# Optimization experiments

Hardware: AMD Instinct MI355X
Metric: run time of the kernel (lower is better)

The kernel has to match this reference:

```python
import jax, jax.numpy as jnp
import numpy as np

CUTOFF = 8.0
N_NODES = 100000
N_EDGES = 3200000
HIDDEN = 256
VOCAB = 178


def _swish(x):
    return x * jax.nn.sigmoid(x)


def _safe_norm(v):
    # L2 norm over last axis with torch-style zero subgradient at 0
    ss = jnp.sum(v * v, axis=-1)
    return jnp.where(ss == 0, 0.0, jnp.sqrt(jnp.where(ss == 0, 1.0, ss)))


def _safe_atan2(b, a):
    # atan2 with finite grad at (0,0); forward value identical (atan2(0,0)=0)
    deg = (a == 0) & (b == 0)
    return jnp.arctan2(b, jnp.where(deg, 1.0, a))


def _scatter_argmin(d, idx, num_seg):
    # replicates torch_scatter.scatter_min argmin output (empty segments -> 0)
    E = d.shape[0]
    mn = jax.ops.segment_min(d, idx, num_segments=num_seg)
    cand = jnp.where(d == mn[idx], jnp.arange(E), E)
    am = jax.ops.segment_min(cand, idx, num_segments=num_seg)
    return jnp.where(am >= E, 0, am)


def _dist_calc(cutoff, vecs, dist, i, j, num_nodes):
    argmin0 = _scatter_argmin(dist, i, num_nodes)
    n0 = j[argmin0]
    dist1 = dist + jnp.zeros_like(dist).at[argmin0].set(cutoff)
    argmin1 = _scatter_argmin(dist1, i, num_nodes)
    n1 = j[argmin1]
    argmin0_j = _scatter_argmin(dist, j, num_nodes)
    n0_j = i[argmin0_j]
    dist1_j = dist + jnp.zeros_like(dist).at[argmin0_j].set(cutoff)
    argmin1_j = _scatter_argmin(dist1_j, j, num_nodes)
    n1_j = i[argmin1_j]

    n0 = n0[i]
    n1 = n1[i]
    n0_j = n0_j[j]
    n1_j = n1_j[j]

    idx_iref = jnp.where(n0 == j, argmin1[i], argmin0[i])
    idx_jref = jnp.where(n0_j == i, argmin1_j[j], argmin0_j[j])

    pos_ji = vecs                      # [E,3]
    pos_in0 = vecs[argmin0[i]]         # vecs[argmin0][i]
    pos_in1 = vecs[argmin1[i]]
    pos_iref = vecs[idx_iref]
    pos_jref_j = vecs[idx_jref]

    a = jnp.sum(-pos_ji * pos_in0, axis=-1)
    b = _safe_norm(jnp.cross(-pos_ji, pos_in0))
    theta = _safe_atan2(b, a)
    theta = jnp.where(theta < 0, theta + jnp.pi, theta)

    dist_ji = _safe_norm(pos_ji)

    plane1 = jnp.cross(-pos_ji, pos_in0)
    plane2 = jnp.cross(-pos_ji, pos_in1)
    a = jnp.sum(plane1 * plane2, axis=-1)
    b = jnp.sum(jnp.cross(plane1, plane2) * pos_ji, axis=-1) / dist_ji
    phi = _safe_atan2(b, a)
    phi = jnp.where(phi < 0, phi + jnp.pi, phi)

    plane1 = jnp.cross(pos_ji, pos_jref_j)
    plane2 = jnp.cross(pos_ji, pos_iref)
    a = jnp.sum(plane1 * plane2, axis=-1)
    b = jnp.sum(jnp.cross(plane1, plane2) * pos_ji, axis=-1) / dist_ji
    tau = _safe_atan2(b, a)
    tau = jnp.where(tau < 0, tau + jnp.pi, tau)

    return dist, theta, phi, tau


def setup_inputs() -> dict:
    key = jax.random.key(0)
    k1, k2, k3, k4, k5 = jax.random.split(key, 5)
    x = jax.random.randint(k1, (N_NODES,), 0, VOCAB)
    pos = jax.random.normal(k2, (N_NODES, 3), jnp.float32) * 3.0
    i = jax.random.randint(k3, (N_EDGES,), 0, N_NODES)
    off = jax.random.randint(k4, (N_EDGES,), 1, N_NODES)
    j = (i + off) % N_NODES  # no self-edges -> dist > 0
    edge_index = jnp.stack([i, j])
    emb_weight = jax.random.normal(k5, (VOCAB, HIDDEN), jnp.float32)
    return {"x": x, "pos": pos, "edge_index": edge_index, "emb_weight": emb_weight}


def reference(x, pos, edge_index, emb_weight):
    i, j = edge_index[0], edge_index[1]
    vecs = pos[j] - pos[i]          # [E,3]
    dist = _safe_norm(vecs)         # [E]
    h = _swish(emb_weight[x])       # [N,H]
    dist, theta, phi, tau = _dist_calc(CUTOFF, vecs, dist, i, j, pos.shape[0])
    return h, dist, theta, phi, tau
```

## Files before the change

### kernel.cpp

```cpp
#include <hip/hip_runtime.h>
#include <math.h>

#define HID 256
#define PI_F 3.14159265358979323846f
typedef unsigned long long ull;

struct F3 { float x, y, z; };

__device__ __forceinline__ F3 crossc(F3 a, F3 b) {
    F3 r;
    float t1 = a.z * b.y;
    r.x = __builtin_fmaf(a.y, b.z, -t1);
    float t2 = a.x * b.z;
    r.y = __builtin_fmaf(a.z, b.x, -t2);
    float t3 = a.y * b.x;
    r.z = __builtin_fmaf(a.x, b.y, -t3);
    return r;
}
__device__ __forceinline__ float dotf(F3 a, F3 b) {
#pragma clang fp contract(off)
    float px = a.x * b.x;
    float py = a.y * b.y;
    float pz = a.z * b.z;
    return (px + py) + pz;
}
__device__ __forceinline__ float sqrt_cr(float ss) {
    return (float)sqrt((double)ss);
}
__device__ __forceinline__ float safe_atan2(float b, float a) {
    float aa = (a == 0.f && b == 0.f) ? 1.f : a;
    return atan2f(b, aa);
}
__device__ __forceinline__ F3 loadp(const float* __restrict__ pos, int n) {
    F3 r;
    r.x = pos[3 * n + 0];
    r.y = pos[3 * n + 1];
    r.z = pos[3 * n + 2];
    return r;
}
__device__ __forceinline__ F3 subv(F3 a, F3 b) {
#pragma clang fp contract(off)
    F3 r;
    r.x = a.x - b.x;
    r.y = a.y - b.y;
    r.z = a.z - b.z;
    return r;
}
__device__ __forceinline__ ull umin64(ull a, ull b) { return a < b ? a : b; }
__device__ __forceinline__ ull umax64(ull a, ull b) { return a > b ? a : b; }

__device__ __forceinline__ void insert2(ull* __restrict__ s, unsigned db, ull key) {
    unsigned hi2 = ((const unsigned*)s)[3];
    if (db > hi2) return;
    unsigned hi1 = ((const unsigned*)s)[1];
    if (db <= hi1) {
        ull ret = atomicMin(&s[0], key);
        ull loser = umax64(ret, key);
        if (loser != ~0ull) atomicMin(&s[1], loser);
    } else {
        atomicMin(&s[1], key);
    }
}

__global__ void k_pass1(const int* __restrict__ ei, const int* __restrict__ ej,
                        const float* __restrict__ pos, float* __restrict__ dist,
                        ull* __restrict__ slotsA, ull* __restrict__ slotsB,
                        const unsigned* __restrict__ thrA, const unsigned* __restrict__ thrB,
                        int e0, int e1) {
#pragma clang fp contract(off)
    int e = e0 + blockIdx.x * blockDim.x + threadIdx.x;
    if (e >= e1) return;
    int ii = ei[e], jj = ej[e];
    F3 v = subv(loadp(pos, jj), loadp(pos, ii));
    float sx = v.x * v.x;
    float sy = v.y * v.y;
    float sz = v.z * v.z;
    float ss = (sx + sy) + sz;
    float d = (ss == 0.f) ? 0.f : sqrt_cr(ss);
    dist[e] = d;
    unsigned db = __float_as_uint(d);
    ull key = ((ull)db << 32) | (unsigned)e;
    if (db <= thrA[ii]) insert2(&slotsA[2 * (size_t)ii], db, key);
    if (db <= thrB[jj]) insert2(&slotsB[2 * (size_t)jj], db, key);
}

__global__ void k_snapshot(const ull* __restrict__ slotsA, const ull* __restrict__ slotsB,
                           unsigned* __restrict__ thrA, unsigned* __restrict__ thrB, int N) {
    int n = blockIdx.x * blockDim.x + threadIdx.x;
    if (n >= N) return;
    thrA[n] = (unsigned)(slotsA[2 * (size_t)n + 1] >> 32);
    thrB[n] = (unsigned)(slotsB[2 * (size_t)n + 1] >> 32);
}

__global__ void k_prep(const ull* __restrict__ slotsA, const ull* __restrict__ slotsB,
                       const int* __restrict__ ei, const int* __restrict__ ej,
                       const float* __restrict__ pos,
                       float4* __restrict__ nodeI, float4* __restrict__ nodeJ,
                       int* __restrict__ a0i, int* __restrict__ a0j,
                       unsigned* __restrict__ flags, int N) {
#pragma clang fp contract(off)
    int n = blockIdx.x * blockDim.x + threadIdx.x;
    if (n >= N) return;

    ull k1 = slotsA[2 * (size_t)n];
    int a0, a1;
    if (k1 == ~0ull) {
        a0 = 0; a1 = 0;
        atomicOr(&flags[0], 1u);
    } else {
        a0 = (int)(k1 & 0xffffffffu);
        float d0 = __uint_as_float((unsigned)(k1 >> 32));
        ull mkey = ((ull)__float_as_uint(d0 + 8.0f) << 32) | (unsigned)a0;
        ull k2 = slotsA[2 * (size_t)n + 1];
        if (k2 == ~0ull) a1 = a0;
        else a1 = (mkey < k2) ? a0 : (int)(k2 & 0xffffffffu);
    }
    a0i[n] = a0;
    F3 in0 = subv(loadp(pos, ej[a0]), loadp(pos, ei[a0]));
    int n0 = ej[a0];
    F3 in1 = subv(loadp(pos, ej[a1]), loadp(pos, ei[a1]));
    nodeI[2 * (size_t)n]     = make_float4(in0.x, in0.y, in0.z, __int_as_float(n0));
    nodeI[2 * (size_t)n + 1] = make_float4(in1.x, in1.y, in1.z, 0.f);

    ull q1 = slotsB[2 * (size_t)n];
    int b0, b1;
    if (q1 == ~0ull) {
        b0 = 0; b1 = 0;
        atomicOr(&flags[1], 1u);
    } else {
        b0 = (int)(q1 & 0xffffffffu);
        float d0 = __uint_as_float((unsigned)(q1 >> 32));
        ull mkey = ((ull)__float_as_uint(d0 + 8.0f) << 32) | (unsigned)b0;
        ull q2 = slotsB[2 * (size_t)n + 1];
        if (q2 == ~0ull) b1 = b0;
        else b1 = (mkey < q2) ? b0 : (int)(q2 & 0xffffffffu);
    }
    a0j[n] = b0;
    F3 w0 = subv(loadp(pos, ej[b0]), loadp(pos, ei[b0]));
    int m0 = ei[b0];
    F3 w1 = subv(loadp(pos, ej[b1]), loadp(pos, ei[b1]));
    nodeJ[2 * (size_t)n]     = make_float4(w0.x, w0.y, w0.z, __int_as_float(m0));
    nodeJ[2 * (size_t)n + 1] = make_float4(w1.x, w1.y, w1.z, 0.f);
}

__global__ void k_fix(const unsigned* __restrict__ flags,
                      const int* __restrict__ ei, const int* __restrict__ ej,
                      const float* __restrict__ dist,
                      const int* __restrict__ a0i, const int* __restrict__ a0j,
                      const float* __restrict__ pos,
                      float4* __restrict__ nodeI, float4* __restrict__ nodeJ, int E) {
#pragma clang fp contract(off)
    __shared__ ull smin[256];
    int side = blockIdx.x;
    if (flags[side] == 0u) return;
    const int* seg = (side == 0) ? ei : ej;
    int s = seg[0];
    int marked = (side == 0) ? a0i[s] : a0j[s];
    ull local = ~0ull;
    for (int e = threadIdx.x; e < E; e += 256) {
        if (seg[e] != s) continue;
        float d = dist[e];
        float dm = (e == marked || e == 0) ? (d + 8.0f) : d;
        ull key = ((ull)__float_as_uint(dm) << 32) | (unsigned)e;
        local = umin64(local, key);
    }
    smin[threadIdx.x] = local;
    __syncthreads();
    for (int w = 128; w > 0; w >>= 1) {
        if (threadIdx.x < w) smin[threadIdx.x] = umin64(smin[threadIdx.x], smin[threadIdx.x + w]);
        __syncthreads();
    }
    if (threadIdx.x == 0) {
        int a1 = (smin[0] == ~0ull) ? 0 : (int)(smin[0] & 0xffffffffu);
        F3 v = subv(loadp(pos, ej[a1]), loadp(pos, ei[a1]));
        if (side == 0) nodeI[2 * (size_t)s + 1] = make_float4(v.x, v.y, v.z, 0.f);
        else           nodeJ[2 * (size_t)s + 1] = make_float4(v.x, v.y, v.z, 0.f);
    }
}

__global__ void k_angles(const int* __restrict__ ei, const int* __restrict__ ej,
                         const float* __restrict__ pos, const float* __restrict__ dist,
                         const float4* __restrict__ nodeI, const float4* __restrict__ nodeJ,
                         float* __restrict__ theta, float* __restrict__ phi,
                         float* __restrict__ tau, int E) {
    int e = blockIdx.x * blockDim.x + threadIdx.x;
    if (e >= E) return;
    int ii = ei[e], jj = ej[e];

    float4 A0 = nodeI[2 * (size_t)ii];
    float4 A1 = nodeI[2 * (size_t)ii + 1];
    float4 B0 = nodeJ[2 * (size_t)jj];
    float4 B1 = nodeJ[2 * (size_t)jj + 1];
    int n0 = __float_as_int(A0.w);
    int m0 = __float_as_int(B0.w);

    F3 in0; in0.x = A0.x; in0.y = A0.y; in0.z = A0.z;
    F3 in1; in1.x = A1.x; in1.y = A1.y; in1.z = A1.z;
    F3 w0;  w0.x = B0.x;  w0.y = B0.y;  w0.z = B0.z;
    F3 w1;  w1.x = B1.x;  w1.y = B1.y;  w1.z = B1.z;

    F3 iref = (n0 == jj) ? in1 : in0;
    F3 jref = (m0 == ii) ? w1 : w0;

    F3 p = subv(loadp(pos, jj), loadp(pos, ii));
    F3 mp;
    mp.x = -p.x; mp.y = -p.y; mp.z = -p.z;

    float a = dotf(mp, in0);
    F3 c1 = crossc(mp, in0);
    float ssb = dotf(c1, c1);
    float b = (ssb == 0.f) ? 0.f : sqrt_cr(ssb);
    float th = safe_atan2(b, a);
    if (th < 0.f) th += PI_F;

    float dji = dist[e];

    F3 pl2 = crossc(mp, in1);
    a = dotf(c1, pl2);
    F3 cc = crossc(c1, pl2);
    b = dotf(cc, p) / dji;
    float ph = safe_atan2(b, a);
    if (ph < 0.f) ph += PI_F;

    F3 t1 = crossc(p, jref);
    F3 t2 = crossc(p, iref);
    a = dotf(t1, t2);
    cc = crossc(t1, t2);
    b = dotf(cc, p) / dji;
    float ta = safe_atan2(b, a);
    if (ta < 0.f) ta += PI_F;

    theta[e] = th;
    phi[e] = ph;
    tau[e] = ta;
}

__global__ void k_embed(const int* __restrict__ x, const float* __restrict__ w,
                        float* __restrict__ h, int total4) {
    int t = blockIdx.x * blockDim.x + threadIdx.x;
    if (t >= total4) return;
    int n = t >> 6;
    int c = t & 63;
    int row = x[n];
    float4 v = *reinterpret_cast<const float4*>(w + (size_t)row * HID + c * 4);
    float4 o;
    o.x = v.x / (1.f + expf(-v.x));
    o.y = v.y / (1.f + expf(-v.y));
    o.z = v.z / (1.f + expf(-v.z));
    o.w = v.w / (1.f + expf(-v.w));
    *reinterpret_cast<float4*>(h + (size_t)n * HID + c * 4) = o;
}

extern "C" void kernel_launch(void* const* d_in, const int* in_sizes, int n_in,
                              void* d_out, int out_size, void* d_ws, size_t ws_size,
                              hipStream_t stream) {
    const int* x = (const int*)d_in[0];
    const float* pos = (const float*)d_in[1];
    const int* eidx = (const int*)d_in[2];
    const float* emb = (const float*)d_in[3];

    const int N = in_sizes[0];
    const int E = in_sizes[2] / 2;
    const int* ei = eidx;
    const int* ej = eidx + E;

    float* out = (float*)d_out;
    float* out_h = out;
    float* out_dist = out + (size_t)N * HID;
    float* out_theta = out_dist + E;
    float* out_phi = out_theta + E;
    float* out_tau = out_phi + E;

    ull* slotsA = (ull*)out_h;
    ull* slotsB = slotsA + 2 * (size_t)N;
    unsigned* thrA = (unsigned*)(slotsB + 2 * (size_t)N);
    unsigned* thrB = thrA + N;
    float4* nodeI = (float4*)(thrB + N);
    float4* nodeJ = nodeI + 2 * (size_t)N;
    int* a0i = (int*)(nodeJ + 2 * (size_t)N);
    int* a0j = a0i + N;
    unsigned* flags = (unsigned*)(a0j + N);

    const int BS = 256;
    int gN = (N + BS - 1) / BS;
    int total4 = N * (HID / 4);
    int gH = (total4 + BS - 1) / BS;

    hipMemsetAsync(slotsA, 0xFF, 4 * (size_t)N * sizeof(ull) + 2 * (size_t)N * sizeof(unsigned), stream);
    hipMemsetAsync(flags, 0, 2 * sizeof(unsigned), stream);

    int c0 = 0, c1 = E / 16, c2 = E / 8, c3 = E / 4, c4 = E / 2, c5 = E;
    int bounds[6] = {c0, c1, c2, c3, c4, c5};
    for (int k = 0; k < 5; k++) {
        int lo = bounds[k], hi = bounds[k + 1];
        if (hi <= lo) continue;
        int g = (hi - lo + BS - 1) / BS;
        k_pass1<<<g, BS, 0, stream>>>(ei, ej, pos, out_dist, slotsA, slotsB,
                                      thrA, thrB, lo, hi);
        if (k < 4)
            k_snapshot<<<gN, BS, 0, stream>>>(slotsA, slotsB, thrA, thrB, N);
    }

    k_prep<<<gN, BS, 0, stream>>>(slotsA, slotsB, ei, ej, pos,
                                  nodeI, nodeJ, a0i, a0j, flags, N);
    k_fix<<<2, BS, 0, stream>>>(flags, ei, ej, out_dist, a0i, a0j, pos,
                                nodeI, nodeJ, E);
    k_angles<<<(E + BS - 1) / BS, BS, 0, stream>>>(ei, ej, pos, out_dist, nodeI, nodeJ,
                                                   out_theta, out_phi, out_tau, E);
    k_embed<<<gH, BS, 0, stream>>>(x, emb, out_h, total4);
}
```

Before: 388.3 us.

## Privatize top-2 atomic slots per XCC and merge in snapshot/prep

Each edge's atomic-min insertion now goes to a per-XCC private copy of the per-node top-2 slots, selected by the hardware XCC id register, using workgroup-scoped relaxed atomics. Snapshot and prep kernels merge the 8 copies to get the global two smallest keys. The aim is to keep atomics local to each die's L2 and avoid cross-die coherence traffic. The edge chunking also drops from 5 chunks to 4. The cost is 8x slot memory, plus a larger memset and more reads in snapshot and prep. Workgroup scope on global memory shared across workgroups on the same XCC depends on L2-level atomic behaviour for correctness.

```diff
diff --git a/kernel.cpp b/kernel.cpp
--- a/kernel.cpp
+++ b/kernel.cpp
@@ -47,29 +47,51 @@
     return r;
 }
 __device__ __forceinline__ ull umin64(ull a, ull b) { return a < b ? a : b; }
-__device__ __forceinline__ ull umax64(ull a, ull b) { return a > b ? a : b; }
-
-__device__ __forceinline__ void insert2(ull* __restrict__ s, unsigned db, ull key) {
+
+__device__ __forceinline__ unsigned xcc_id() {
+    return __builtin_amdgcn_s_getreg((3u << 11) | 20u) & 7u;
+}
+
+__device__ __forceinline__ void insert2_loc(ull* __restrict__ s, unsigned db, ull key) {
     unsigned hi2 = ((const unsigned*)s)[3];
     if (db > hi2) return;
     unsigned hi1 = ((const unsigned*)s)[1];
     if (db <= hi1) {
-        ull ret = atomicMin(&s[0], key);
-        ull loser = umax64(ret, key);
-        if (loser != ~0ull) atomicMin(&s[1], loser);
+        ull ret = __hip_atomic_fetch_min(&s[0], key, __ATOMIC_RELAXED,
+                                         __HIP_MEMORY_SCOPE_WORKGROUP);
+        ull loser = ret > key ? ret : key;
+        if (loser != ~0ull)
+            __hip_atomic_fetch_min(&s[1], loser, __ATOMIC_RELAXED,
+                                   __HIP_MEMORY_SCOPE_WORKGROUP);
     } else {
-        atomicMin(&s[1], key);
+        __hip_atomic_fetch_min(&s[1], key, __ATOMIC_RELAXED,
+                               __HIP_MEMORY_SCOPE_WORKGROUP);
+    }
+}
+
+__device__ __forceinline__ void merge8(const ull* __restrict__ slots8, size_t twoN,
+                                       int n, ull& m1, ull& m2) {
+    m1 = ~0ull; m2 = ~0ull;
+#pragma unroll
+    for (int c = 0; c < 8; c++) {
+        ull a = slots8[(size_t)c * twoN + 2 * (size_t)n];
+        ull b = slots8[(size_t)c * twoN + 2 * (size_t)n + 1];
+        if (a < m1) { m2 = m1; m1 = a; } else if (a < m2) m2 = a;
+        if (b < m1) { m2 = m1; m1 = b; } else if (b < m2) m2 = b;
     }
 }
 
 __global__ void k_pass1(const int* __restrict__ ei, const int* __restrict__ ej,
                         const float* __restrict__ pos, float* __restrict__ dist,
-                        ull* __restrict__ slotsA, ull* __restrict__ slotsB,
+                        ull* __restrict__ slots8A, ull* __restrict__ slots8B,
                         const unsigned* __restrict__ thrA, const unsigned* __restrict__ thrB,
-                        int e0, int e1) {
+                        size_t twoN, int e0, int e1) {
 #pragma clang fp contract(off)
     int e = e0 + blockIdx.x * blockDim.x + threadIdx.x;
     if (e >= e1) return;
+    unsigned c = xcc_id();
+    ull* sA = slots8A + (size_t)c * twoN;
+    ull* sB = slots8B + (size_t)c * twoN;
     int ii = ei[e], jj = ej[e];
     F3 v = subv(loadp(pos, jj), loadp(pos, ii));
     float sx = v.x * v.x;
@@ -80,29 +102,34 @@
     dist[e] = d;
     unsigned db = __float_as_uint(d);
     ull key = ((ull)db << 32) | (unsigned)e;
-    if (db <= thrA[ii]) insert2(&slotsA[2 * (size_t)ii], db, key);
-    if (db <= thrB[jj]) insert2(&slotsB[2 * (size_t)jj], db, key);
-}
-
-__global__ void k_snapshot(const ull* __restrict__ slotsA, const ull* __restrict__ slotsB,
-                           unsigned* __restrict__ thrA, unsigned* __restrict__ thrB, int N) {
+    if (db <= thrA[ii]) insert2_loc(&sA[2 * (size_t)ii], db, key);
+    if (db <= thrB[jj]) insert2_loc(&sB[2 * (size_t)jj], db, key);
+}
+
+__global__ void k_snapshot(const ull* __restrict__ slots8A, const ull* __restrict__ slots8B,
+                           unsigned* __restrict__ thrA, unsigned* __restrict__ thrB,
+                           size_t twoN, int N) {
     int n = blockIdx.x * blockDim.x + threadIdx.x;
     if (n >= N) return;
-    thrA[n] = (unsigned)(slotsA[2 * (size_t)n + 1] >> 32);
-    thrB[n] = (unsigned)(slotsB[2 * (size_t)n + 1] >> 32);
-}
-
-__global__ void k_prep(const ull* __restrict__ slotsA, const ull* __restrict__ slotsB,
+    ull m1, m2;
+    merge8(slots8A, twoN, n, m1, m2);
+    thrA[n] = (unsigned)(m2 >> 32);
+    merge8(slots8B, twoN, n, m1, m2);
+    thrB[n] = (unsigned)(m2 >> 32);
+}
+
+__global__ void k_prep(const ull* __restrict__ slots8A, const ull* __restrict__ slots8B,
                        const int* __restrict__ ei, const int* __restrict__ ej,
                        const float* __restrict__ pos,
                        float4* __restrict__ nodeI, float4* __restrict__ nodeJ,
                        int* __restrict__ a0i, int* __restrict__ a0j,
-                       unsigned* __restrict__ flags, int N) {
+                       unsigned* __restrict__ flags, size_t twoN, int N) {
 #pragma clang fp contract(off)
     int n = blockIdx.x * blockDim.x + threadIdx.x;
     if (n >= N) return;
 
-    ull k1 = slotsA[2 * (size_t)n];
+    ull k1, k2;
+    merge8(slots8A, twoN, n, k1, k2);
     int a0, a1;
     if (k1 == ~0ull) {
         a0 = 0; a1 = 0;
@@ -111,7 +138,6 @@
         a0 = (int)(k1 & 0xffffffffu);
         float d0 = __uint_as_float((unsigned)(k1 >> 32));
         ull mkey = ((ull)__float_as_uint(d0 + 8.0f) << 32) | (unsigned)a0;
-        ull k2 = slotsA[2 * (size_t)n + 1];
         if (k2 == ~0ull) a1 = a0;
         else a1 = (mkey < k2) ? a0 : (int)(k2 & 0xffffffffu);
     }
@@ -122,7 +148,8 @@
     nodeI[2 * (size_t)n]     = make_float4(in0.x, in0.y, in0.z, __int_as_float(n0));
     nodeI[2 * (size_t)n + 1] = make_float4(in1.x, in1.y, in1.z, 0.f);
 
-    ull q1 = slotsB[2 * (size_t)n];
+    ull q1, q2;
+    merge8(slots8B, twoN, n, q1, q2);
     int b0, b1;
     if (q1 == ~0ull) {
         b0 = 0; b1 = 0;
@@ -131,7 +158,6 @@
         b0 = (int)(q1 & 0xffffffffu);
         float d0 = __uint_as_float((unsigned)(q1 >> 32));
         ull mkey = ((ull)__float_as_uint(d0 + 8.0f) << 32) | (unsigned)b0;
-        ull q2 = slotsB[2 * (size_t)n + 1];
         if (q2 == ~0ull) b1 = b0;
         else b1 = (mkey < q2) ? b0 : (int)(q2 & 0xffffffffu);
     }
@@ -271,13 +297,14 @@
     float* out_phi = out_theta + E;
     float* out_tau = out_phi + E;
 
-    ull* slotsA = (ull*)out_h;
-    ull* slotsB = slotsA + 2 * (size_t)N;
-    unsigned* thrA = (unsigned*)(slotsB + 2 * (size_t)N);
+    size_t twoN = 2 * (size_t)N;
+    ull* slots8A = (ull*)out_h;
+    ull* slots8B = slots8A + 8 * twoN;
+    unsigned* thrA = (unsigned*)(slots8B + 8 * twoN);
     unsigned* thrB = thrA + N;
     float4* nodeI = (float4*)(thrB + N);
-    float4* nodeJ = nodeI + 2 * (size_t)N;
-    int* a0i = (int*)(nodeJ + 2 * (size_t)N);
+    float4* nodeJ = nodeI + twoN;
+    int* a0i = (int*)(nodeJ + twoN);
     int* a0j = a0i + N;
     unsigned* flags = (unsigned*)(a0j + N);
 
@@ -286,23 +313,22 @@
     int total4 = N * (HID / 4);
     int gH = (total4 + BS - 1) / BS;
 
-    hipMemsetAsync(slotsA, 0xFF, 4 * (size_t)N * sizeof(ull) + 2 * (size_t)N * sizeof(unsigned), stream);
+    hipMemsetAsync(slots8A, 0xFF, 16 * twoN * sizeof(ull) + 2 * (size_t)N * sizeof(unsigned), stream);
     hipMemsetAsync(flags, 0, 2 * sizeof(unsigned), stream);
 
-    int c0 = 0, c1 = E / 16, c2 = E / 8, c3 = E / 4, c4 = E / 2, c5 = E;
-    int bounds[6] = {c0, c1, c2, c3, c4, c5};
-    for (int k = 0; k < 5; k++) {
+    int bounds[5] = {0, E / 8, E / 4, E / 2, E};
+    for (int k = 0; k < 4; k++) {
         int lo = bounds[k], hi = bounds[k + 1];
         if (hi <= lo) continue;
         int g = (hi - lo + BS - 1) / BS;
-        k_pass1<<<g, BS, 0, stream>>>(ei, ej, pos, out_dist, slotsA, slotsB,
-                                      thrA, thrB, lo, hi);
-        if (k < 4)
-            k_snapshot<<<gN, BS, 0, stream>>>(slotsA, slotsB, thrA, thrB, N);
-    }
-
-    k_prep<<<gN, BS, 0, stream>>>(slotsA, slotsB, ei, ej, pos,
-                                  nodeI, nodeJ, a0i, a0j, flags, N);
+        k_pass1<<<g, BS, 0, stream>>>(ei, ej, pos, out_dist, slots8A, slots8B,
+                                      thrA, thrB, twoN, lo, hi);
+        if (k < 3)
+            k_snapshot<<<gN, BS, 0, stream>>>(slots8A, slots8B, thrA, thrB, twoN, N);
+    }
+
+    k_prep<<<gN, BS, 0, stream>>>(slots8A, slots8B, ei, ej, pos,
+                                  nodeI, nodeJ, a0i, a0j, flags, twoN, N);
     k_fix<<<2, BS, 0, stream>>>(flags, ei, ej, out_dist, a0i, a0j, pos,
                                 nodeI, nodeJ, E);
     k_angles<<<(E + BS - 1) / BS, BS, 0, stream>>>(ei, ej, pos, out_dist, nodeI, nodeJ,
```

Measured after the change: 389.7 us. Within noise of the previous version (+0.4%).
